# Kernel tuning notes

Hardware: AMD Instinct MI355X
Metric: run time of the kernel (lower is better)

Reference implementation:

```python
import jax, jax.numpy as jnp
import numpy as np


def _compute_deltas(ts, m):
    """Affine time-decay recurrence: delta_0 = 0; for t>=1:
    delta_t = gap_t + (1 - m_{t-1}) * delta_{t-1}, with gap broadcast over features.
    ts: [b, s] timestamps, m: [b, s, f] float 0/1 mask. Returns [b, s, f]."""
    b, s, f = m.shape
    gaps = ts[:, 1:] - ts[:, :-1]          # [b, s-1]
    a = 1.0 - m[:, :-1, :]                 # [b, s-1, f] decay coefficient

    def step(d, inp):
        g_t, a_t = inp                      # g_t: [b], a_t: [b, f]
        d = g_t[:, None] + a_t * d
        return d, d

    gT = jnp.swapaxes(gaps, 0, 1)          # [s-1, b]
    aT = jnp.swapaxes(a, 0, 1)             # [s-1, b, f]
    _, ds = jax.lax.scan(step, jnp.zeros((b, f), ts.dtype), (gT, aT))
    ds = jnp.swapaxes(ds, 0, 1)            # [b, s-1, f]
    return jnp.concatenate([jnp.zeros((b, 1, f), ts.dtype), ds], axis=1)


def setup_inputs() -> dict:
    key = jax.random.key(0)
    k1, k2, k3 = jax.random.split(key, 3)
    b, s, f = 32, 2048, 768
    # monotonically increasing timestamps (cumsum of positive gaps)
    gaps = jax.random.uniform(k1, (b, s), minval=1.0, maxval=60.0, dtype=jnp.float32)
    timestamps = jnp.cumsum(gaps, axis=1)
    encoded_data = jax.random.normal(k2, (b, s, f), dtype=jnp.float32)
    masks = jax.random.randint(k3, (b, s, f), 0, 2, dtype=jnp.int32)
    return {"timestamps": timestamps, "encoded_data": encoded_data, "masks": masks}


def reference(timestamps, encoded_data, masks):
    """JAX translation of _prepare_brits_data. Returns stacked
    [forward_deltas, backward_deltas, backward_X] of shape [3, b, s, f].
    (forward X / masks are pass-through inputs; backward mask is flip(masks).)"""
    m = masks.astype(timestamps.dtype)
    forward_deltas = _compute_deltas(timestamps, m)
    ts_b = jnp.flip(timestamps, axis=1)
    m_b = jnp.flip(m, axis=1)
    backward_deltas = jnp.abs(_compute_deltas(ts_b, m_b))
    x_b = jnp.flip(encoded_data, axis=1)
    return jnp.stack([forward_deltas, backward_deltas, x_b], axis=0)
```

## Files before the change

### kernel.cpp

```cpp
#include <hip/hip_runtime.h>
#include <stdint.h>

static constexpr int B = 32, S = 2048, F = 768;
static constexpr int CS = 64;
static constexpr int NCH = S / CS;
static constexpr int F4 = F / 4;
static constexpr int FT = F4;

typedef float v4f __attribute__((ext_vector_type(4)));
typedef int   v4i __attribute__((ext_vector_type(4)));
typedef unsigned int v4u __attribute__((ext_vector_type(4)));

__device__ __forceinline__ v4f mk4(float a, float b, float c, float d) {
    v4f v; v.x = a; v.y = b; v.z = c; v.w = d; return v;
}

__global__ __launch_bounds__(FT) void passA(const v4i* __restrict__ masks,
                                            uint32_t* __restrict__ bw) {
    const int blk = blockIdx.x;
    const int b = blk >> 5, c = blk & 31;
    const int j = threadIdx.x;
    const v4i* mp = masks + (size_t)(b * S + c * CS) * F4 + j;
    uint32_t a0 = 0, a1 = 0, a2 = 0, a3 = 0;
    uint32_t c0 = 0, c1 = 0, c2 = 0, c3 = 0;
    #pragma unroll
    for (int g = 0; g < 8; ++g) {
        v4i mv[8];
        #pragma unroll
        for (int q = 0; q < 8; ++q) mv[q] = __builtin_nontemporal_load(&mp[(size_t)(g * 8 + q) * F4]);
        #pragma unroll
        for (int q = 0; q < 8; ++q) {
            const int k = g * 8 + q;
            const uint32_t bit = 1u << (k & 31);
            if (k < 32) {
                if (mv[q].x) a0 |= bit;
                if (mv[q].y) a1 |= bit;
                if (mv[q].z) a2 |= bit;
                if (mv[q].w) a3 |= bit;
            } else {
                if (mv[q].x) c0 |= bit;
                if (mv[q].y) c1 |= bit;
                if (mv[q].z) c2 |= bit;
                if (mv[q].w) c3 |= bit;
            }
        }
    }
    v4u w0; w0.x = a0; w0.y = c0; w0.z = a1; w0.w = c1;
    v4u w1; w1.x = a2; w1.y = c2; w1.z = a3; w1.w = c3;
    v4u* dst = reinterpret_cast<v4u*>(bw + ((size_t)blk * F + 4 * j) * 2);
    dst[0] = w0;
    dst[1] = w1;
}

__global__ __launch_bounds__(FT) void passC(const float* __restrict__ ts,
                                            const uint32_t* __restrict__ bw,
                                            float* __restrict__ out) {
    const int blk = blockIdx.x;
    const int b = blk >> 5, c = blk & 31;
    const int g0 = c * CS;
    const int j = threadIdx.x;
    const size_t N4 = (size_t)B * S * F4;
    const float* tsb = ts + (size_t)b * S;

    __shared__ float tss[CS];
    if (j < CS) tss[j] = tsb[g0 + j];
    __syncthreads();

    const v4u* own = reinterpret_cast<const v4u*>(bw + ((size_t)blk * F + 4 * j) * 2);
    v4u w0 = own[0], w1 = own[1];
    uint32_t alo[4] = {w0.x, w0.z, w1.x, w1.z};
    uint32_t ahi[4] = {w0.y, w0.w, w1.y, w1.w};

    float p[4], n[4];
    {
        float def = tsb[0];
        p[0] = p[1] = p[2] = p[3] = def;
        uint32_t need = 0xFu;
        for (int d = c - 1; d >= 0 && need; --d) {
            const v4u* nb = reinterpret_cast<const v4u*>(bw + ((size_t)(b * NCH + d) * F + 4 * j) * 2);
            v4u u0 = nb[0], u1 = nb[1];
            uint32_t lo[4] = {u0.x, u0.z, u1.x, u1.z};
            uint32_t hi[4] = {u0.y, u0.w, u1.y, u1.w};
            const int base = d * CS;
            #pragma unroll
            for (int i = 0; i < 4; ++i) if (need & (1u << i)) {
                if (hi[i])      { p[i] = tsb[base + 32 + (31 - __clz((int)hi[i]))]; need &= ~(1u << i); }
                else if (lo[i]) { p[i] = tsb[base +      (31 - __clz((int)lo[i]))]; need &= ~(1u << i); }
            }
        }
    }
    {
        float def = tsb[S - 1];
        n[0] = n[1] = n[2] = n[3] = def;
        uint32_t need = 0xFu;
        for (int d = c + 1; d < NCH && need; ++d) {
            const v4u* nb = reinterpret_cast<const v4u*>(bw + ((size_t)(b * NCH + d) * F + 4 * j) * 2);
            v4u u0 = nb[0], u1 = nb[1];
            uint32_t lo[4] = {u0.x, u0.z, u1.x, u1.z};
            uint32_t hi[4] = {u0.y, u0.w, u1.y, u1.w};
            const int base = d * CS;
            #pragma unroll
            for (int i = 0; i < 4; ++i) if (need & (1u << i)) {
                if (lo[i])      { n[i] = tsb[base +      (__ffs((int)lo[i]) - 1)]; need &= ~(1u << i); }
                else if (hi[i]) { n[i] = tsb[base + 32 + (__ffs((int)hi[i]) - 1)]; need &= ~(1u << i); }
            }
        }
    }

    v4f* o0 = reinterpret_cast<v4f*>(out) + (size_t)(b * S + g0) * F4 + j;
    #pragma unroll
    for (int k = 0; k < 32; ++k) {
        float t = tss[k];
        __builtin_nontemporal_store(mk4(t - p[0], t - p[1], t - p[2], t - p[3]), &o0[(size_t)k * F4]);
        const uint32_t bit = 1u << k;
        #pragma unroll
        for (int i = 0; i < 4; ++i) if (alo[i] & bit) p[i] = t;
    }
    #pragma unroll
    for (int k = 32; k < 64; ++k) {
        float t = tss[k];
        __builtin_nontemporal_store(mk4(t - p[0], t - p[1], t - p[2], t - p[3]), &o0[(size_t)k * F4]);
        const uint32_t bit = 1u << (k - 32);
        #pragma unroll
        for (int i = 0; i < 4; ++i) if (ahi[i] & bit) p[i] = t;
    }

    v4f* o1b = reinterpret_cast<v4f*>(out) + N4 + (size_t)b * S * F4 + j;
    #pragma unroll
    for (int k = 63; k >= 32; --k) {
        float t = tss[k];
        size_t fr = (size_t)(S - 1 - g0 - k) * F4;
        __builtin_nontemporal_store(mk4(n[0] - t, n[1] - t, n[2] - t, n[3] - t), &o1b[fr]);
        const uint32_t bit = 1u << (k - 32);
        #pragma unroll
        for (int i = 0; i < 4; ++i) if (ahi[i] & bit) n[i] = t;
    }
    #pragma unroll
    for (int k = 31; k >= 0; --k) {
        float t = tss[k];
        size_t fr = (size_t)(S - 1 - g0 - k) * F4;
        __builtin_nontemporal_store(mk4(n[0] - t, n[1] - t, n[2] - t, n[3] - t), &o1b[fr]);
        const uint32_t bit = 1u << k;
        #pragma unroll
        for (int i = 0; i < 4; ++i) if (alo[i] & bit) n[i] = t;
    }
}

static constexpr int CPY_BLOCKS = 2048;
__global__ __launch_bounds__(256) void copyK(const v4f* __restrict__ x,
                                             v4f* __restrict__ o2) {
    const size_t N4 = (size_t)B * S * F4;
    const size_t stride = (size_t)CPY_BLOCKS * 256;
    for (size_t i = (size_t)blockIdx.x * 256 + threadIdx.x; i < N4; i += stride) {
        size_t row = i / F4;
        size_t f   = i - row * F4;
        size_t t   = row & (S - 1);
        size_t src = (row - t + (S - 1 - t)) * F4 + f;
        __builtin_nontemporal_store(__builtin_nontemporal_load(&x[src]), &o2[i]);
    }
}

__global__ __launch_bounds__(FT) void deltaProbeK(const float* __restrict__ ts,
                                                  const int4* __restrict__ masks,
                                                  float* __restrict__ out) {
    const int pair = blockIdx.x;
    const int b = pair >> 5, sc = pair & 31;
    const int g0 = sc * CS;
    const int j = threadIdx.x;
    const size_t N4 = (size_t)B * S * F4;
    const float* tsb = ts + (size_t)b * S;
    const int4* mbase = masks + (size_t)b * S * F4 + j;
    __shared__ float tss[CS];
    if (j < CS) tss[j] = tsb[g0 + j];
    __syncthreads();
    uint32_t a0 = 0, a1 = 0, a2 = 0, a3 = 0, c0 = 0, c1 = 0, c2 = 0, c3 = 0;
    #pragma unroll
    for (int g = 0; g < 8; ++g) {
        int4 mv[8];
        #pragma unroll
        for (int q = 0; q < 8; ++q) mv[q] = mbase[(size_t)(g0 + g * 8 + q) * F4];
        #pragma unroll
        for (int q = 0; q < 8; ++q) {
            const int k = g * 8 + q;
            const uint32_t bit = 1u << (k & 31);
            if (k < 32) { if (mv[q].x) a0 |= bit; if (mv[q].y) a1 |= bit; if (mv[q].z) a2 |= bit; if (mv[q].w) a3 |= bit; }
            else        { if (mv[q].x) c0 |= bit; if (mv[q].y) c1 |= bit; if (mv[q].z) c2 |= bit; if (mv[q].w) c3 |= bit; }
        }
    }
    float t0v = tsb[0];
    float p0 = t0v, p1 = t0v, p2 = t0v, p3 = t0v;
    if (g0 > 0) {
        unsigned um = 0xFu; int r = g0 - 1;
        while (um && r >= 0) {
            int rl = (r - 7 > 0) ? r - 7 : 0; int nn = r - rl + 1;
            int4 mv[8];
            #pragma unroll
            for (int q = 0; q < 8; ++q) if (q < nn) mv[q] = mbase[(size_t)(r - q) * F4];
            #pragma unroll
            for (int q = 0; q < 8; ++q) if (q < nn) {
                float t = tsb[r - q];
                if ((um & 1u) && mv[q].x) { p0 = t; um &= ~1u; }
                if ((um & 2u) && mv[q].y) { p1 = t; um &= ~2u; }
                if ((um & 4u) && mv[q].z) { p2 = t; um &= ~4u; }
                if ((um & 8u) && mv[q].w) { p3 = t; um &= ~8u; }
            }
            r = rl - 1;
        }
    }
    float tev = tsb[S - 1];
    float n0 = tev, n1 = tev, n2 = tev, n3 = tev;
    if (g0 + CS < S) {
        unsigned um = 0xFu; int r = g0 + CS;
        while (um && r < S) {
            int rh = (r + 7 < S - 1) ? r + 7 : S - 1; int nn = rh - r + 1;
            int4 mv[8];
            #pragma unroll
            for (int q = 0; q < 8; ++q) if (q < nn) mv[q] = mbase[(size_t)(r + q) * F4];
            #pragma unroll
            for (int q = 0; q < 8; ++q) if (q < nn) {
                float t = tsb[r + q];
                if ((um & 1u) && mv[q].x) { n0 = t; um &= ~1u; }
                if ((um & 2u) && mv[q].y) { n1 = t; um &= ~2u; }
                if ((um & 4u) && mv[q].z) { n2 = t; um &= ~4u; }
                if ((um & 8u) && mv[q].w) { n3 = t; um &= ~8u; }
            }
            r = rh + 1;
        }
    }
    v4f* o0 = reinterpret_cast<v4f*>(out) + (size_t)(b * S + g0) * F4 + j;
    #pragma unroll
    for (int k = 0; k < 32; ++k) {
        float t = tss[k];
        __builtin_nontemporal_store(mk4(t - p0, t - p1, t - p2, t - p3), &o0[(size_t)k * F4]);
        const uint32_t bit = 1u << k;
        if (a0 & bit) p0 = t; if (a1 & bit) p1 = t; if (a2 & bit) p2 = t; if (a3 & bit) p3 = t;
    }
    #pragma unroll
    for (int k = 32; k < 64; ++k) {
        float t = tss[k];
        __builtin_nontemporal_store(mk4(t - p0, t - p1, t - p2, t - p3), &o0[(size_t)k * F4]);
        const uint32_t bit = 1u << (k - 32);
        if (c0 & bit) p0 = t; if (c1 & bit) p1 = t; if (c2 & bit) p2 = t; if (c3 & bit) p3 = t;
    }
    v4f* o1b = reinterpret_cast<v4f*>(out) + N4 + (size_t)b * S * F4 + j;
    #pragma unroll
    for (int k = 63; k >= 32; --k) {
        float t = tss[k];
        size_t fr = (size_t)(S - 1 - g0 - k) * F4;
        __builtin_nontemporal_store(mk4(n0 - t, n1 - t, n2 - t, n3 - t), &o1b[fr]);
        const uint32_t bit = 1u << (k - 32);
        if (c0 & bit) n0 = t; if (c1 & bit) n1 = t; if (c2 & bit) n2 = t; if (c3 & bit) n3 = t;
    }
    #pragma unroll
    for (int k = 31; k >= 0; --k) {
        float t = tss[k];
        size_t fr = (size_t)(S - 1 - g0 - k) * F4;
        __builtin_nontemporal_store(mk4(n0 - t, n1 - t, n2 - t, n3 - t), &o1b[fr]);
        const uint32_t bit = 1u << k;
        if (a0 & bit) n0 = t; if (a1 & bit) n1 = t; if (a2 & bit) n2 = t; if (a3 & bit) n3 = t;
    }
}

extern "C" void kernel_launch(void* const* d_in, const int* in_sizes, int n_in,
                              void* d_out, int out_size, void* d_ws, size_t ws_size,
                              hipStream_t stream) {
    const float* ts    = (const float*)d_in[0];
    const v4f* x       = (const v4f*)d_in[1];
    float* out = (float*)d_out;
    const size_t N4 = (size_t)B * S * F4;
    const size_t bw_bytes = (size_t)B * NCH * F * 2 * sizeof(uint32_t);

    if (ws_size >= bw_bytes) {
        uint32_t* bw = (uint32_t*)d_ws;
        passA<<<B * NCH, FT, 0, stream>>>((const v4i*)d_in[2], bw);
        passC<<<B * NCH, FT, 0, stream>>>(ts, bw, out);
    } else {
        deltaProbeK<<<B * NCH, FT, 0, stream>>>(ts, (const int4*)d_in[2], out);
    }
    copyK<<<CPY_BLOCKS, 256, 0, stream>>>(x, reinterpret_cast<v4f*>(out) + 2 * N4);
}
```

Measured before the change: 193.8 us.

## Fuse flip-copy into mask-pack and delta kernels via interleaved copy blocks

```diff
diff --git a/kernel.cpp b/kernel.cpp
--- a/kernel.cpp
+++ b/kernel.cpp
@@ -6,6 +6,7 @@
 static constexpr int NCH = S / CS;
 static constexpr int F4 = F / 4;
 static constexpr int FT = F4;
+static constexpr int CP1 = 48;
 
 typedef float v4f __attribute__((ext_vector_type(4)));
 typedef int   v4i __attribute__((ext_vector_type(4)));
@@ -15,12 +16,30 @@
     v4f v; v.x = a; v.y = b; v.z = c; v.w = d; return v;
 }
 
-__global__ __launch_bounds__(FT) void passA(const v4i* __restrict__ masks,
-                                            uint32_t* __restrict__ bw) {
+__global__ __launch_bounds__(FT) void kD1(const v4i* __restrict__ masks,
+                                          const v4f* __restrict__ x,
+                                          uint32_t* __restrict__ bw,
+                                          float* __restrict__ out) {
     const int blk = blockIdx.x;
-    const int b = blk >> 5, c = blk & 31;
+    const int pair = blk >> 1;
+    const int b = pair >> 5, c = pair & 31;
+    const int g0 = c * CS;
     const int j = threadIdx.x;
-    const v4i* mp = masks + (size_t)(b * S + c * CS) * F4 + j;
+    const size_t N4 = (size_t)B * S * F4;
+
+    if (blk & 1) {
+        const v4f* xb = x + (size_t)b * S * F4 + j;
+        v4f* o2 = reinterpret_cast<v4f*>(out) + 2 * N4 + (size_t)(b * S + g0) * F4 + j;
+        #pragma unroll 8
+        for (int k = 0; k < CP1; ++k) {
+            __builtin_nontemporal_store(
+                __builtin_nontemporal_load(&xb[(size_t)(S - 1 - g0 - k) * F4]),
+                &o2[(size_t)k * F4]);
+        }
+        return;
+    }
+
+    const v4i* mp = masks + (size_t)(b * S + g0) * F4 + j;
     uint32_t a0 = 0, a1 = 0, a2 = 0, a3 = 0;
     uint32_t c0 = 0, c1 = 0, c2 = 0, c3 = 0;
     #pragma unroll
@@ -47,26 +66,40 @@
     }
     v4u w0; w0.x = a0; w0.y = c0; w0.z = a1; w0.w = c1;
     v4u w1; w1.x = a2; w1.y = c2; w1.z = a3; w1.w = c3;
-    v4u* dst = reinterpret_cast<v4u*>(bw + ((size_t)blk * F + 4 * j) * 2);
+    v4u* dst = reinterpret_cast<v4u*>(bw + ((size_t)pair * F + 4 * j) * 2);
     dst[0] = w0;
     dst[1] = w1;
 }
 
-__global__ __launch_bounds__(FT) void passC(const float* __restrict__ ts,
-                                            const uint32_t* __restrict__ bw,
-                                            float* __restrict__ out) {
+__global__ __launch_bounds__(FT) void kD2(const float* __restrict__ ts,
+                                          const uint32_t* __restrict__ bw,
+                                          const v4f* __restrict__ x,
+                                          float* __restrict__ out) {
     const int blk = blockIdx.x;
-    const int b = blk >> 5, c = blk & 31;
+    const int pair = blk >> 1;
+    const int b = pair >> 5, c = pair & 31;
     const int g0 = c * CS;
     const int j = threadIdx.x;
     const size_t N4 = (size_t)B * S * F4;
+
+    if (blk & 1) {
+        const v4f* xb = x + (size_t)b * S * F4 + j;
+        v4f* o2 = reinterpret_cast<v4f*>(out) + 2 * N4 + (size_t)(b * S + g0) * F4 + j;
+        #pragma unroll 8
+        for (int k = CP1; k < CS; ++k) {
+            __builtin_nontemporal_store(
+                __builtin_nontemporal_load(&xb[(size_t)(S - 1 - g0 - k) * F4]),
+                &o2[(size_t)k * F4]);
+        }
+        return;
+    }
+
     const float* tsb = ts + (size_t)b * S;
-
     __shared__ float tss[CS];
     if (j < CS) tss[j] = tsb[g0 + j];
     __syncthreads();
 
-    const v4u* own = reinterpret_cast<const v4u*>(bw + ((size_t)blk * F + 4 * j) * 2);
+    const v4u* own = reinterpret_cast<const v4u*>(bw + ((size_t)pair * F + 4 * j) * 2);
     v4u w0 = own[0], w1 = own[1];
     uint32_t alo[4] = {w0.x, w0.z, w1.x, w1.z};
     uint32_t ahi[4] = {w0.y, w0.w, w1.y, w1.w};
@@ -146,6 +179,107 @@
     }
 }
 
+__global__ __launch_bounds__(FT) void deltaProbeK(const float* __restrict__ ts,
+                                                  const int4* __restrict__ masks,
+                                                  float* __restrict__ out) {
+    const int pair = blockIdx.x;
+    const int b = pair >> 5, sc = pair & 31;
+    const int g0 = sc * CS;
+    const int j = threadIdx.x;
+    const size_t N4 = (size_t)B * S * F4;
+    const float* tsb = ts + (size_t)b * S;
+    const int4* mbase = masks + (size_t)b * S * F4 + j;
+    __shared__ float tss[CS];
+    if (j < CS) tss[j] = tsb[g0 + j];
+    __syncthreads();
+    uint32_t a0 = 0, a1 = 0, a2 = 0, a3 = 0, c0 = 0, c1 = 0, c2 = 0, c3 = 0;
+    #pragma unroll
+    for (int g = 0; g < 8; ++g) {
+        int4 mv[8];
+        #pragma unroll
+        for (int q = 0; q < 8; ++q) mv[q] = mbase[(size_t)(g0 + g * 8 + q) * F4];
+        #pragma unroll
+        for (int q = 0; q < 8; ++q) {
+            const int k = g * 8 + q;
+            const uint32_t bit = 1u << (k & 31);
+            if (k < 32) { if (mv[q].x) a0 |= bit; if (mv[q].y) a1 |= bit; if (mv[q].z) a2 |= bit; if (mv[q].w) a3 |= bit; }
+            else        { if (mv[q].x) c0 |= bit; if (mv[q].y) c1 |= bit; if (mv[q].z) c2 |= bit; if (mv[q].w) c3 |= bit; }
+        }
+    }
+    float t0v = tsb[0];
+    float p0 = t0v, p1 = t0v, p2 = t0v, p3 = t0v;
+    if (g0 > 0) {
+        unsigned um = 0xFu; int r = g0 - 1;
+        while (um && r >= 0) {
+            int rl = (r - 7 > 0) ? r - 7 : 0; int nn = r - rl + 1;
+            int4 mv[8];
+            #pragma unroll
+            for (int q = 0; q < 8; ++q) if (q < nn) mv[q] = mbase[(size_t)(r - q) * F4];
+            #pragma unroll
+            for (int q = 0; q < 8; ++q) if (q < nn) {
+                float t = tsb[r - q];
+                if ((um & 1u) && mv[q].x) { p0 = t; um &= ~1u; }
+                if ((um & 2u) && mv[q].y) { p1 = t; um &= ~2u; }
+                if ((um & 4u) && mv[q].z) { p2 = t; um &= ~4u; }
+                if ((um & 8u) && mv[q].w) { p3 = t; um &= ~8u; }
+            }
+            r = rl - 1;
+        }
+    }
+    float tev = tsb[S - 1];
+    float n0 = tev, n1 = tev, n2 = tev, n3 = tev;
+    if (g0 + CS < S) {
+        unsigned um = 0xFu; int r = g0 + CS;
+        while (um && r < S) {
+            int rh = (r + 7 < S - 1) ? r + 7 : S - 1; int nn = rh - r + 1;
+            int4 mv[8];
+            #pragma unroll
+            for (int q = 0; q < 8; ++q) if (q < nn) mv[q] = mbase[(size_t)(r + q) * F4];
+            #pragma unroll
+            for (int q = 0; q < 8; ++q) if (q < nn) {
+                float t = tsb[r + q];
+                if ((um & 1u) && mv[q].x) { n0 = t; um &= ~1u; }
+                if ((um & 2u) && mv[q].y) { n1 = t; um &= ~2u; }
+                if ((um & 4u) && mv[q].z) { n2 = t; um &= ~4u; }
+                if ((um & 8u) && mv[q].w) { n3 = t; um &= ~8u; }
+            }
+            r = rh + 1;
+        }
+    }
+    v4f* o0 = reinterpret_cast<v4f*>(out) + (size_t)(b * S + g0) * F4 + j;
+    #pragma unroll
+    for (int k = 0; k < 32; ++k) {
+        float t = tss[k];
+        __builtin_nontemporal_store(mk4(t - p0, t - p1, t - p2, t - p3), &o0[(size_t)k * F4]);
+        const uint32_t bit = 1u << k;
+        if (a0 & bit) p0 = t; if (a1 & bit) p1 = t; if (a2 & bit) p2 = t; if (a3 & bit) p3 = t;
+    }
+    #pragma unroll
+    for (int k = 32; k < 64; ++k) {
+        float t = tss[k];
+        __builtin_nontemporal_store(mk4(t - p0, t - p1, t - p2, t - p3), &o0[(size_t)k * F4]);
+        const uint32_t bit = 1u << (k - 32);
+        if (c0 & bit) p0 = t; if (c1 & bit) p1 = t; if (c2 & bit) p2 = t; if (c3 & bit) p3 = t;
+    }
+    v4f* o1b = reinterpret_cast<v4f*>(out) + N4 + (size_t)b * S * F4 + j;
+    #pragma unroll
+    for (int k = 63; k >= 32; --k) {
+        float t = tss[k];
+        size_t fr = (size_t)(S - 1 - g0 - k) * F4;
+        __builtin_nontemporal_store(mk4(n0 - t, n1 - t, n2 - t, n3 - t), &o1b[fr]);
+        const uint32_t bit = 1u << (k - 32);
+        if (c0 & bit) n0 = t; if (c1 & bit) n1 = t; if (c2 & bit) n2 = t; if (c3 & bit) n3 = t;
+    }
+    #pragma unroll
+    for (int k = 31; k >= 0; --k) {
+        float t = tss[k];
+        size_t fr = (size_t)(S - 1 - g0 - k) * F4;
+        __builtin_nontemporal_store(mk4(n0 - t, n1 - t, n2 - t, n3 - t), &o1b[fr]);
+        const uint32_t bit = 1u << k;
+        if (a0 & bit) n0 = t; if (a1 & bit) n1 = t; if (a2 & bit) n2 = t; if (a3 & bit) n3 = t;
+    }
+}
+
 static constexpr int CPY_BLOCKS = 2048;
 __global__ __launch_bounds__(256) void copyK(const v4f* __restrict__ x,
                                              v4f* __restrict__ o2) {
@@ -160,107 +294,6 @@
     }
 }
 
-__global__ __launch_bounds__(FT) void deltaProbeK(const float* __restrict__ ts,
-                                                  const int4* __restrict__ masks,
-                                                  float* __restrict__ out) {
-    const int pair = blockIdx.x;
-    const int b = pair >> 5, sc = pair & 31;
-    const int g0 = sc * CS;
-    const int j = threadIdx.x;
-    const size_t N4 = (size_t)B * S * F4;
-    const float* tsb = ts + (size_t)b * S;
-    const int4* mbase = masks + (size_t)b * S * F4 + j;
-    __shared__ float tss[CS];
-    if (j < CS) tss[j] = tsb[g0 + j];
-    __syncthreads();
-    uint32_t a0 = 0, a1 = 0, a2 = 0, a3 = 0, c0 = 0, c1 = 0, c2 = 0, c3 = 0;
-    #pragma unroll
-    for (int g = 0; g < 8; ++g) {
-        int4 mv[8];
-        #pragma unroll
-        for (int q = 0; q < 8; ++q) mv[q] = mbase[(size_t)(g0 + g * 8 + q) * F4];
-        #pragma unroll
-        for (int q = 0; q < 8; ++q) {
-            const int k = g * 8 + q;
-            const uint32_t bit = 1u << (k & 31);
-            if (k < 32) { if (mv[q].x) a0 |= bit; if (mv[q].y) a1 |= bit; if (mv[q].z) a2 |= bit; if (mv[q].w) a3 |= bit; }
-            else        { if (mv[q].x) c0 |= bit; if (mv[q].y) c1 |= bit; if (mv[q].z) c2 |= bit; if (mv[q].w) c3 |= bit; }
-        }
-    }
-    float t0v = tsb[0];
-    float p0 = t0v, p1 = t0v, p2 = t0v, p3 = t0v;
-    if (g0 > 0) {
-        unsigned um = 0xFu; int r = g0 - 1;
-        while (um && r >= 0) {
-            int rl = (r - 7 > 0) ? r - 7 : 0; int nn = r - rl + 1;
-            int4 mv[8];
-            #pragma unroll
-            for (int q = 0; q < 8; ++q) if (q < nn) mv[q] = mbase[(size_t)(r - q) * F4];
-            #pragma unroll
-            for (int q = 0; q < 8; ++q) if (q < nn) {
-                float t = tsb[r - q];
-                if ((um & 1u) && mv[q].x) { p0 = t; um &= ~1u; }
-                if ((um & 2u) && mv[q].y) { p1 = t; um &= ~2u; }
-                if ((um & 4u) && mv[q].z) { p2 = t; um &= ~4u; }
-                if ((um & 8u) && mv[q].w) { p3 = t; um &= ~8u; }
-            }
-            r = rl - 1;
-        }
-    }
-    float tev = tsb[S - 1];
-    float n0 = tev, n1 = tev, n2 = tev, n3 = tev;
-    if (g0 + CS < S) {
-        unsigned um = 0xFu; int r = g0 + CS;
-        while (um && r < S) {
-            int rh = (r + 7 < S - 1) ? r + 7 : S - 1; int nn = rh - r + 1;
-            int4 mv[8];
-            #pragma unroll
-            for (int q = 0; q < 8; ++q) if (q < nn) mv[q] = mbase[(size_t)(r + q) * F4];
-            #pragma unroll
-            for (int q = 0; q < 8; ++q) if (q < nn) {
-                float t = tsb[r + q];
-                if ((um & 1u) && mv[q].x) { n0 = t; um &= ~1u; }
-                if ((um & 2u) && mv[q].y) { n1 = t; um &= ~2u; }
-                if ((um & 4u) && mv[q].z) { n2 = t; um &= ~4u; }
-                if ((um & 8u) && mv[q].w) { n3 = t; um &= ~8u; }
-            }
-            r = rh + 1;
-        }
-    }
-    v4f* o0 = reinterpret_cast<v4f*>(out) + (size_t)(b * S + g0) * F4 + j;
-    #pragma unroll
-    for (int k = 0; k < 32; ++k) {
-        float t = tss[k];
-        __builtin_nontemporal_store(mk4(t - p0, t - p1, t - p2, t - p3), &o0[(size_t)k * F4]);
-        const uint32_t bit = 1u << k;
-        if (a0 & bit) p0 = t; if (a1 & bit) p1 = t; if (a2 & bit) p2 = t; if (a3 & bit) p3 = t;
-    }
-    #pragma unroll
-    for (int k = 32; k < 64; ++k) {
-        float t = tss[k];
-        __builtin_nontemporal_store(mk4(t - p0, t - p1, t - p2, t - p3), &o0[(size_t)k * F4]);
-        const uint32_t bit = 1u << (k - 32);
-        if (c0 & bit) p0 = t; if (c1 & bit) p1 = t; if (c2 & bit) p2 = t; if (c3 & bit) p3 = t;
-    }
-    v4f* o1b = reinterpret_cast<v4f*>(out) + N4 + (size_t)b * S * F4 + j;
-    #pragma unroll
-    for (int k = 63; k >= 32; --k) {
-        float t = tss[k];
-        size_t fr = (size_t)(S - 1 - g0 - k) * F4;
-        __builtin_nontemporal_store(mk4(n0 - t, n1 - t, n2 - t, n3 - t), &o1b[fr]);
-        const uint32_t bit = 1u << (k - 32);
-        if (c0 & bit) n0 = t; if (c1 & bit) n1 = t; if (c2 & bit) n2 = t; if (c3 & bit) n3 = t;
-    }
-    #pragma unroll
-    for (int k = 31; k >= 0; --k) {
-        float t = tss[k];
-        size_t fr = (size_t)(S - 1 - g0 - k) * F4;
-        __builtin_nontemporal_store(mk4(n0 - t, n1 - t, n2 - t, n3 - t), &o1b[fr]);
-        const uint32_t bit = 1u << k;
-        if (a0 & bit) n0 = t; if (a1 & bit) n1 = t; if (a2 & bit) n2 = t; if (a3 & bit) n3 = t;
-    }
-}
-
 extern "C" void kernel_launch(void* const* d_in, const int* in_sizes, int n_in,
                               void* d_out, int out_size, void* d_ws, size_t ws_size,
                               hipStream_t stream) {
@@ -272,10 +305,10 @@
 
     if (ws_size >= bw_bytes) {
         uint32_t* bw = (uint32_t*)d_ws;
-        passA<<<B * NCH, FT, 0, stream>>>((const v4i*)d_in[2], bw);
-        passC<<<B * NCH, FT, 0, stream>>>(ts, bw, out);
+        kD1<<<2 * B * NCH, FT, 0, stream>>>((const v4i*)d_in[2], x, bw, out);
+        kD2<<<2 * B * NCH, FT, 0, stream>>>(ts, bw, x, out);
     } else {
         deltaProbeK<<<B * NCH, FT, 0, stream>>>(ts, (const int4*)d_in[2], out);
-    }
-    copyK<<<CPY_BLOCKS, 256, 0, stream>>>(x, reinterpret_cast<v4f*>(out) + 2 * N4);
-}
+        copyK<<<CPY_BLOCKS, 256, 0, stream>>>(x, reinterpret_cast<v4f*>(out) + 2 * N4);
+    }
+}
```

New measurement: 207.4 us. +7.0%, slower.
